# Optimization experiments

Hardware: AMD Instinct MI355X
Metric: run time of the kernel (lower is better)

Reference implementation:

```python
import jax, jax.numpy as jnp
import numpy as np

N_NODES = 100000
N_EDGES = 3200000
IN_DIM = 256
HID_DIM = 64


def setup_inputs() -> dict:
    key = jax.random.key(0)
    k1, k2, k3 = jax.random.split(key, 3)
    x = jax.random.normal(k1, (N_NODES, IN_DIM), dtype=jnp.float32)
    edge_index = jax.random.randint(k2, (2, N_EDGES), 0, N_NODES, dtype=jnp.int32)
    # Glorot-ish init for the GCN weight
    W = jax.random.normal(k3, (IN_DIM, HID_DIM), dtype=jnp.float32) * (1.0 / np.sqrt(IN_DIM))
    b = jnp.zeros((HID_DIM,), dtype=jnp.float32)
    return {"x": x, "edge_index": edge_index, "W": W, "b": b}


def reference(x, edge_index, W, b):
    N = x.shape[0]
    # --- gcn_norm: add self loops, symmetric degree normalization ---
    loop = jnp.arange(N, dtype=edge_index.dtype)
    row = jnp.concatenate([edge_index[0], loop])  # source nodes
    col = jnp.concatenate([edge_index[1], loop])  # destination nodes
    deg = jax.ops.segment_sum(jnp.ones(row.shape[0], dtype=x.dtype), col, num_segments=N)
    dinv = jnp.where(deg > 0, jax.lax.rsqrt(deg), 0.0)
    norm = dinv[row] * dinv[col]  # [E+N]
    # --- linear transform first (in_dim > out_dim), then aggregate ---
    xt = x @ W  # [N, hid]
    msg = xt[row] * norm[:, None]  # [E+N, hid] gathered messages
    out = jax.ops.segment_sum(msg, col, num_segments=N) + b
    return jax.nn.relu(out)
```

## Files before the change

kernel.cpp:

```cpp
#include <hip/hip_runtime.h>

#define IN_DIM 256
#define HID 64
#define SBSH 8
#define SBN 256
#define NSB_MAX 512
#define PB 256

static __device__ __forceinline__ unsigned bf16r(float f) {
    unsigned x = __float_as_uint(f);
    return (x + 0x7fffu + ((x >> 16) & 1u)) >> 16;
}

static __device__ __forceinline__ float blo(unsigned u) { return __uint_as_float(u << 16); }
static __device__ __forceinline__ float bhi(unsigned u) { return __uint_as_float(u & 0xffff0000u); }

__global__ void __launch_bounds__(256) k_zero(int* __restrict__ p, int n) {
    int i = blockIdx.x * 256 + threadIdx.x;
    if (i < n) p[i] = 0;
}

__global__ void __launch_bounds__(256) k_p2a(const int* __restrict__ col,
                                             int* __restrict__ bucketCnt,
                                             int* __restrict__ blkHist, int E, int nsb) {
    __shared__ int hist[NSB_MAX];
    const int tid = threadIdx.x, b = blockIdx.x;
    const int chunkE = (E + PB - 1) / PB;
    const int s = b * chunkE, e = min(s + chunkE, E);
    for (int i = tid; i < nsb; i += 256) hist[i] = 0;
    __syncthreads();
    for (int j = s + tid; j < e; j += 256) atomicAdd(&hist[col[j] >> SBSH], 1);
    __syncthreads();
    for (int i = tid; i < nsb; i += 256) {
        int h = hist[i];
        blkHist[i * PB + b] = h;
        if (h) atomicAdd(&bucketCnt[i], h);
    }
}

__global__ void __launch_bounds__(256) k_scanB(const int* __restrict__ bucketCnt,
                                               int* __restrict__ bucketOff,
                                               int* __restrict__ rowptr,
                                               int nsb, int N, int E) {
    __shared__ int tmp[256];
    const int tid = threadIdx.x;
    const int PT = (nsb + 255) >> 8;
    int v[8];
    int s = 0;
    for (int k = 0; k < PT; ++k) {
        int i = tid * PT + k;
        v[k] = (i < nsb) ? bucketCnt[i] : 0;
        s += v[k];
    }
    tmp[tid] = s;
    __syncthreads();
    for (int d = 1; d < 256; d <<= 1) {
        int val = (tid >= d) ? tmp[tid - d] : 0;
        __syncthreads();
        tmp[tid] += val;
        __syncthreads();
    }
    int run = tmp[tid] - s;
    for (int k = 0; k < PT; ++k) {
        int i = tid * PT + k;
        if (i < nsb) bucketOff[i] = run;
        run += v[k];
    }
    if (tid == 255) { bucketOff[nsb] = E; rowptr[N] = E; }
}

__global__ void __launch_bounds__(256) k_scanBlk(const int* __restrict__ bucketOff,
                                                 const int* __restrict__ blkHist,
                                                 int* __restrict__ blkCur) {
    __shared__ int tmp[PB];
    const int i = blockIdx.x, t = threadIdx.x;
    int v = blkHist[i * PB + t];
    tmp[t] = v;
    __syncthreads();
    for (int d = 1; d < PB; d <<= 1) {
        int val = (t >= d) ? tmp[t - d] : 0;
        __syncthreads();
        tmp[t] += val;
        __syncthreads();
    }
    blkCur[i * PB + t] = bucketOff[i] + tmp[t] - v;
}

__global__ void __launch_bounds__(256) k_p2b(const int* __restrict__ row,
                                             const int* __restrict__ col,
                                             const int* __restrict__ blkCur,
                                             int* __restrict__ part, int E, int nsb) {
    __shared__ int lcur[NSB_MAX];
    const int tid = threadIdx.x, b = blockIdx.x;
    const int chunkE = (E + PB - 1) / PB;
    const int s = b * chunkE, e = min(s + chunkE, E);
    for (int i = tid; i < nsb; i += 256) lcur[i] = blkCur[i * PB + b];
    __syncthreads();
    for (int j = s + tid; j < e; j += 256) {
        int c = col[j];
        int pos = atomicAdd(&lcur[c >> SBSH], 1);
        part[pos] = (row[j] << SBSH) | (c & (SBN - 1));
    }
}

__global__ void __launch_bounds__(256) k_sortb(const int* __restrict__ bucketOff,
                                               const int* __restrict__ part,
                                               int* __restrict__ rowptr,
                                               float* __restrict__ dinv,
                                               int* __restrict__ eRow, int N) {
    __shared__ int hcnt[SBN];
    __shared__ int tmp[SBN];
    __shared__ int cur[SBN];
    const int tid = threadIdx.x;
    const int base = blockIdx.x << SBSH;
    const int s = bucketOff[blockIdx.x];
    const int e = bucketOff[blockIdx.x + 1];

    hcnt[tid] = 0;
    __syncthreads();
    for (int j = s + tid; j < e; j += 256) atomicAdd(&hcnt[part[j] & (SBN - 1)], 1);
    __syncthreads();
    const int c = hcnt[tid];
    tmp[tid] = c;
    __syncthreads();
    for (int d = 1; d < 256; d <<= 1) {
        int val = (tid >= d) ? tmp[tid - d] : 0;
        __syncthreads();
        tmp[tid] += val;
        __syncthreads();
    }
    const int myBase = s + tmp[tid] - c;
    cur[tid] = myBase;
    const int n = base + tid;
    if (n < N) {
        rowptr[n] = myBase;
        dinv[n] = __frsqrt_rn((float)(c + 1));
    }
    __syncthreads();
    for (int j = s + tid; j < e; j += 256) {
        int p = part[j];
        int pos = atomicAdd(&cur[p & (SBN - 1)], 1);
        eRow[pos] = p >> SBSH;
    }
}

__global__ void __launch_bounds__(256) k_gemm(const float* __restrict__ x,
                                              const float* __restrict__ W,
                                              const float* __restrict__ dinv,
                                              unsigned* __restrict__ xsb, int N) {
    __shared__ float xT[32][260];
    __shared__ float Wl[32][64];
    const int t = threadIdx.x;
    const int tmI = t >> 3;
    const int tnI = t & 7;
    const int nodeBase = blockIdx.x * 256;

    float acc[8][8] = {};

    for (int k0 = 0; k0 < IN_DIM; k0 += 32) {
#pragma unroll
        for (int i = 0; i < 2; ++i) {
            int flat = i * 256 + t;
            float4 wv = ((const float4*)W)[k0 * 16 + flat];
            *(float4*)&Wl[flat >> 4][(flat & 15) << 2] = wv;
        }
#pragma unroll
        for (int i = 0; i < 8; ++i) {
            int flat = i * 256 + t;
            int n = flat >> 3;
            int kq = (flat & 7) << 2;
            int gn = nodeBase + n;
            if (gn >= N) gn = N - 1;
            float4 v = *(const float4*)(x + (size_t)gn * IN_DIM + k0 + kq);
            xT[kq + 0][n] = v.x;
            xT[kq + 1][n] = v.y;
            xT[kq + 2][n] = v.z;
            xT[kq + 3][n] = v.w;
        }
        __syncthreads();
#pragma unroll
        for (int k = 0; k < 32; ++k) {
            float xv[8], wv[8];
            *(float4*)&xv[0] = *(const float4*)&xT[k][tmI * 8];
            *(float4*)&xv[4] = *(const float4*)&xT[k][tmI * 8 + 4];
            *(float4*)&wv[0] = *(const float4*)&Wl[k][tnI * 8];
            *(float4*)&wv[4] = *(const float4*)&Wl[k][tnI * 8 + 4];
#pragma unroll
            for (int mi = 0; mi < 8; ++mi)
#pragma unroll
                for (int ni = 0; ni < 8; ++ni)
                    acc[mi][ni] = fmaf(xv[mi], wv[ni], acc[mi][ni]);
        }
        __syncthreads();
    }

#pragma unroll
    for (int mi = 0; mi < 8; ++mi) {
        int n = nodeBase + tmI * 8 + mi;
        if (n < N) {
            float d = dinv[n];
            uint4 o;
            o.x = bf16r(acc[mi][0] * d) | (bf16r(acc[mi][1] * d) << 16);
            o.y = bf16r(acc[mi][2] * d) | (bf16r(acc[mi][3] * d) << 16);
            o.z = bf16r(acc[mi][4] * d) | (bf16r(acc[mi][5] * d) << 16);
            o.w = bf16r(acc[mi][6] * d) | (bf16r(acc[mi][7] * d) << 16);
            *(uint4*)(xsb + (size_t)n * (HID / 2) + tnI * 4) = o;
        }
    }
}

__global__ void __launch_bounds__(256) k_agg(const int* __restrict__ rowptr,
                                             const int* __restrict__ eRow,
                                             const unsigned* __restrict__ xsb,
                                             const float* __restrict__ dinv,
                                             const float* __restrict__ bias,
                                             float* __restrict__ out, int N) {
    const int lane = threadIdx.x & 63;
    const int l = lane & 31;
    const int n = (blockIdx.x * 4 + (threadIdx.x >> 6)) * 2 + (lane >> 5);
    if (n >= N) return;

    const int s = rowptr[n];
    const int e = rowptr[n + 1];

    unsigned u = xsb[(size_t)n * 32 + l];
    float ax = blo(u), ay = bhi(u);
    float b0x = 0.f, b0y = 0.f, b1x = 0.f, b1y = 0.f;
    float b2x = 0.f, b2y = 0.f, b3x = 0.f, b3y = 0.f;
    int j = s;
    for (; j + 7 < e; j += 8) {
        int r0 = eRow[j],     r1 = eRow[j + 1], r2 = eRow[j + 2], r3 = eRow[j + 3];
        int r4 = eRow[j + 4], r5 = eRow[j + 5], r6 = eRow[j + 6], r7 = eRow[j + 7];
        unsigned u0 = xsb[(size_t)r0 * 32 + l];
        unsigned u1 = xsb[(size_t)r1 * 32 + l];
        unsigned u2 = xsb[(size_t)r2 * 32 + l];
        unsigned u3 = xsb[(size_t)r3 * 32 + l];
        unsigned u4 = xsb[(size_t)r4 * 32 + l];
        unsigned u5 = xsb[(size_t)r5 * 32 + l];
        unsigned u6 = xsb[(size_t)r6 * 32 + l];
        unsigned u7 = xsb[(size_t)r7 * 32 + l];
        b0x += blo(u0); b0y += bhi(u0);
        b1x += blo(u1); b1y += bhi(u1);
        b2x += blo(u2); b2y += bhi(u2);
        b3x += blo(u3); b3y += bhi(u3);
        b0x += blo(u4); b0y += bhi(u4);
        b1x += blo(u5); b1y += bhi(u5);
        b2x += blo(u6); b2y += bhi(u6);
        b3x += blo(u7); b3y += bhi(u7);
    }
    for (; j + 3 < e; j += 4) {
        int r0 = eRow[j], r1 = eRow[j + 1], r2 = eRow[j + 2], r3 = eRow[j + 3];
        unsigned u0 = xsb[(size_t)r0 * 32 + l];
        unsigned u1 = xsb[(size_t)r1 * 32 + l];
        unsigned u2 = xsb[(size_t)r2 * 32 + l];
        unsigned u3 = xsb[(size_t)r3 * 32 + l];
        b0x += blo(u0); b0y += bhi(u0);
        b1x += blo(u1); b1y += bhi(u1);
        b2x += blo(u2); b2y += bhi(u2);
        b3x += blo(u3); b3y += bhi(u3);
    }
    for (; j < e; ++j) {
        unsigned u0 = xsb[(size_t)eRow[j] * 32 + l];
        ax += blo(u0); ay += bhi(u0);
    }
    ax += (b0x + b1x) + (b2x + b3x);
    ay += (b0y + b1y) + (b2y + b3y);

    const float d = dinv[n];
    const float2 bl = *(const float2*)&bias[2 * l];
    float2 o;
    o.x = fmaxf(fmaf(ax, d, bl.x), 0.f);
    o.y = fmaxf(fmaf(ay, d, bl.y), 0.f);
    *(float2*)(out + (size_t)n * HID + 2 * l) = o;
}

extern "C" void kernel_launch(void* const* d_in, const int* in_sizes, int n_in,
                              void* d_out, int out_size, void* d_ws, size_t ws_size,
                              hipStream_t stream) {
    const float* x  = (const float*)d_in[0];
    const int*   ei = (const int*)d_in[1];
    const float* W  = (const float*)d_in[2];
    const float* b  = (const float*)d_in[3];
    float* out = (float*)d_out;

    const int N = in_sizes[0] / IN_DIM;
    const int E = in_sizes[1] / 2;
    const int* row = ei;
    const int* col = ei + E;
    const int NSB = (N + SBN - 1) >> SBSH;

    int*      bucketCnt = (int*)d_ws;
    int*      bucketOff = bucketCnt + NSB;
    int*      rowptr    = bucketOff + NSB + 1;
    float*    dinv      = (float*)(rowptr + N + 1);
    unsigned* xsb       = (unsigned*)(dinv + N);
    int*      part      = (int*)(xsb + (size_t)N * (HID / 2));
    int*      eRow      = part + E;
    int*      blkHist   = eRow + E;
    int*      blkCur    = blkHist + NSB * PB;

    k_zero<<<(NSB + 255) / 256, 256, 0, stream>>>(bucketCnt, NSB);
    k_p2a<<<PB, 256, 0, stream>>>(col, bucketCnt, blkHist, E, NSB);
    k_scanB<<<1, 256, 0, stream>>>(bucketCnt, bucketOff, rowptr, NSB, N, E);
    k_scanBlk<<<NSB, PB, 0, stream>>>(bucketOff, blkHist, blkCur);
    k_p2b<<<PB, 256, 0, stream>>>(row, col, blkCur, part, E, NSB);
    k_sortb<<<NSB, 256, 0, stream>>>(bucketOff, part, rowptr, dinv, eRow, N);
    k_gemm<<<(N + 255) / 256, 256, 0, stream>>>(x, W, dinv, xsb, N);
    k_agg<<<(N + 7) / 8, 256, 0, stream>>>(rowptr, eRow, xsb, dinv, b, out, N);
}
```

Measured before the change: 401.5 us.

## Slice bf16 feature table by column groups and aggregate per slice

The GEMM now writes the transformed features in a column-sliced layout: 8 slices of 8 bf16 values, each slice a contiguous table of N×16 bytes. Aggregation launches one block set per slice, so each gather touches a smaller table that fits better in cache. Within a wave, 16 edge groups of 4 lanes gather in parallel and the partial sums are combined with cross-lane shuffles. In exchange, eRow and rowptr are read 8 times, and each gather moves only 16 bytes.

Result: slower. 544.5 us (+35.6%).

```diff
diff --git a/kernel.cpp b/kernel.cpp
--- a/kernel.cpp
+++ b/kernel.cpp
@@ -6,6 +6,7 @@
 #define SBN 256
 #define NSB_MAX 512
 #define PB 256
+#define NSLICE 8
 
 static __device__ __forceinline__ unsigned bf16r(float f) {
     unsigned x = __float_as_uint(f);
@@ -204,74 +205,51 @@
             o.y = bf16r(acc[mi][2] * d) | (bf16r(acc[mi][3] * d) << 16);
             o.z = bf16r(acc[mi][4] * d) | (bf16r(acc[mi][5] * d) << 16);
             o.w = bf16r(acc[mi][6] * d) | (bf16r(acc[mi][7] * d) << 16);
-            *(uint4*)(xsb + (size_t)n * (HID / 2) + tnI * 4) = o;
-        }
-    }
-}
-
-__global__ void __launch_bounds__(256) k_agg(const int* __restrict__ rowptr,
-                                             const int* __restrict__ eRow,
-                                             const unsigned* __restrict__ xsb,
-                                             const float* __restrict__ dinv,
-                                             const float* __restrict__ bias,
-                                             float* __restrict__ out, int N) {
-    const int lane = threadIdx.x & 63;
-    const int l = lane & 31;
-    const int n = (blockIdx.x * 4 + (threadIdx.x >> 6)) * 2 + (lane >> 5);
+            *(uint4*)(xsb + ((size_t)tnI * N + n) * 4) = o;
+        }
+    }
+}
+
+__global__ void __launch_bounds__(256) k_aggs(const int* __restrict__ rowptr,
+                                              const int* __restrict__ eRow,
+                                              const unsigned* __restrict__ xsb,
+                                              const float* __restrict__ dinv,
+                                              const float* __restrict__ bias,
+                                              float* __restrict__ out, int N) {
+    const int slice = blockIdx.x & (NSLICE - 1);
+    const int n = (blockIdx.x >> 3) * 4 + (threadIdx.x >> 6);
     if (n >= N) return;
-
-    const int s = rowptr[n];
-    const int e = rowptr[n + 1];
-
-    unsigned u = xsb[(size_t)n * 32 + l];
-    float ax = blo(u), ay = bhi(u);
-    float b0x = 0.f, b0y = 0.f, b1x = 0.f, b1y = 0.f;
-    float b2x = 0.f, b2y = 0.f, b3x = 0.f, b3y = 0.f;
-    int j = s;
-    for (; j + 7 < e; j += 8) {
-        int r0 = eRow[j],     r1 = eRow[j + 1], r2 = eRow[j + 2], r3 = eRow[j + 3];
-        int r4 = eRow[j + 4], r5 = eRow[j + 5], r6 = eRow[j + 6], r7 = eRow[j + 7];
-        unsigned u0 = xsb[(size_t)r0 * 32 + l];
-        unsigned u1 = xsb[(size_t)r1 * 32 + l];
-        unsigned u2 = xsb[(size_t)r2 * 32 + l];
-        unsigned u3 = xsb[(size_t)r3 * 32 + l];
-        unsigned u4 = xsb[(size_t)r4 * 32 + l];
-        unsigned u5 = xsb[(size_t)r5 * 32 + l];
-        unsigned u6 = xsb[(size_t)r6 * 32 + l];
-        unsigned u7 = xsb[(size_t)r7 * 32 + l];
-        b0x += blo(u0); b0y += bhi(u0);
-        b1x += blo(u1); b1y += bhi(u1);
-        b2x += blo(u2); b2y += bhi(u2);
-        b3x += blo(u3); b3y += bhi(u3);
-        b0x += blo(u4); b0y += bhi(u4);
-        b1x += blo(u5); b1y += bhi(u5);
-        b2x += blo(u6); b2y += bhi(u6);
-        b3x += blo(u7); b3y += bhi(u7);
-    }
-    for (; j + 3 < e; j += 4) {
-        int r0 = eRow[j], r1 = eRow[j + 1], r2 = eRow[j + 2], r3 = eRow[j + 3];
-        unsigned u0 = xsb[(size_t)r0 * 32 + l];
-        unsigned u1 = xsb[(size_t)r1 * 32 + l];
-        unsigned u2 = xsb[(size_t)r2 * 32 + l];
-        unsigned u3 = xsb[(size_t)r3 * 32 + l];
-        b0x += blo(u0); b0y += bhi(u0);
-        b1x += blo(u1); b1y += bhi(u1);
-        b2x += blo(u2); b2y += bhi(u2);
-        b3x += blo(u3); b3y += bhi(u3);
-    }
-    for (; j < e; ++j) {
-        unsigned u0 = xsb[(size_t)eRow[j] * 32 + l];
-        ax += blo(u0); ay += bhi(u0);
-    }
-    ax += (b0x + b1x) + (b2x + b3x);
-    ay += (b0y + b1y) + (b2y + b3y);
-
-    const float d = dinv[n];
-    const float2 bl = *(const float2*)&bias[2 * l];
-    float2 o;
-    o.x = fmaxf(fmaf(ax, d, bl.x), 0.f);
-    o.y = fmaxf(fmaf(ay, d, bl.y), 0.f);
-    *(float2*)(out + (size_t)n * HID + 2 * l) = o;
+    const int j = threadIdx.x & 63;
+    const int g = j >> 2;
+    const int q = j & 3;
+    const unsigned* tab = xsb + (size_t)slice * N * 4;
+
+    const int s = rowptr[n], e = rowptr[n + 1];
+    float sx = 0.f, sy = 0.f;
+    for (int base = s; base < e; base += 16) {
+        int idx = base + g;
+        unsigned u = 0;
+        if (idx < e) {
+            int r = eRow[idx];
+            u = tab[(size_t)r * 4 + q];
+        }
+        sx += blo(u); sy += bhi(u);
+    }
+#pragma unroll
+    for (int m = 4; m < 64; m <<= 1) {
+        sx += __shfl_xor(sx, m, 64);
+        sy += __shfl_xor(sy, m, 64);
+    }
+    if (j < 4) {
+        unsigned us = tab[(size_t)n * 4 + q];
+        sx += blo(us); sy += bhi(us);
+        const float d = dinv[n];
+        const float2 bl = *(const float2*)&bias[slice * 8 + q * 2];
+        float2 o;
+        o.x = fmaxf(fmaf(sx, d, bl.x), 0.f);
+        o.y = fmaxf(fmaf(sy, d, bl.y), 0.f);
+        *(float2*)(out + (size_t)n * HID + slice * 8 + q * 2) = o;
+    }
 }
 
 extern "C" void kernel_launch(void* const* d_in, const int* in_sizes, int n_in,
@@ -306,5 +284,5 @@
     k_p2b<<<PB, 256, 0, stream>>>(row, col, blkCur, part, E, NSB);
     k_sortb<<<NSB, 256, 0, stream>>>(bucketOff, part, rowptr, dinv, eRow, N);
     k_gemm<<<(N + 255) / 256, 256, 0, stream>>>(x, W, dinv, xsb, N);
-    k_agg<<<(N + 7) / 8, 256, 0, stream>>>(rowptr, eRow, xsb, dinv, b, out, N);
-}
+    k_aggs<<<((N + 3) / 4) * NSLICE, 256, 0, stream>>>(rowptr, eRow, xsb, dinv, b, out, N);
+}
```
